# Performance work log

Hardware: AMD Instinct MI355X
Metric: run time of the kernel (lower is better)

## Reference

```python
import jax, jax.numpy as jnp
import numpy as np


def _lstm_cell(x, h, c, w_ih, w_hh, b_ih, b_hh):
    # PyTorch LSTMCell gate order: i, f, g, o
    z = x @ w_ih.T + h @ w_hh.T + b_ih + b_hh
    i, f, g, o = jnp.split(z, 4, axis=-1)
    c_new = jax.nn.sigmoid(f) * c + jax.nn.sigmoid(i) * jnp.tanh(g)
    h_new = jax.nn.sigmoid(o) * jnp.tanh(c_new)
    return h_new, c_new


def setup_inputs() -> dict:
    B, T_in, T_out = 32, 512, 512
    n_mel, n_frames = 80, 1
    n_enc, n_att, n_filt, K = 512, 128, 32, 31
    n_arnn, n_drnn, n_pre = 1024, 1024, 256
    keys = jax.random.split(jax.random.key(0), 25)
    r = lambda k, *s: jax.random.normal(keys[k], s, dtype=jnp.float32) * 0.05
    return {
        "memory": jax.random.normal(keys[0], (B, T_in, n_enc), dtype=jnp.float32),
        "decoder_inputs": jax.random.normal(keys[1], (B, n_mel, T_out), dtype=jnp.float32),
        "memory_lengths": jax.random.randint(keys[2], (B,), T_in // 2, T_in + 1).astype(jnp.int32),
        "prenet_w1": r(3, n_pre, n_mel * n_frames),
        "prenet_w2": r(4, n_pre, n_pre),
        "arnn_w_ih": r(5, 4 * n_arnn, n_pre + n_enc),
        "arnn_w_hh": r(6, 4 * n_arnn, n_arnn),
        "arnn_b_ih": r(7, 4 * n_arnn),
        "arnn_b_hh": r(8, 4 * n_arnn),
        "query_w": r(9, n_att, n_arnn),
        "memory_w": r(10, n_att, n_enc),
        "v_w": r(11, 1, n_att),
        "loc_conv_w": r(12, n_filt, 2, K),
        "loc_dense_w": r(13, n_att, n_filt),
        "drnn_w_ih": r(14, 4 * n_drnn, n_arnn + n_enc),
        "drnn_w_hh": r(15, 4 * n_drnn, n_drnn),
        "drnn_b_ih": r(16, 4 * n_drnn),
        "drnn_b_hh": r(17, 4 * n_drnn),
        "proj_w": r(18, n_mel * n_frames, n_drnn + n_enc),
        "proj_b": r(19, n_mel * n_frames),
        "gate_w": r(20, 1, n_drnn + n_enc),
        "gate_b": r(21, 1),
    }


def reference(memory, decoder_inputs, memory_lengths, prenet_w1, prenet_w2,
              arnn_w_ih, arnn_w_hh, arnn_b_ih, arnn_b_hh,
              query_w, memory_w, v_w, loc_conv_w, loc_dense_w,
              drnn_w_ih, drnn_w_hh, drnn_b_ih, drnn_b_hh,
              proj_w, proj_b, gate_w, gate_b):
    B, T_in, n_enc = memory.shape
    n_mel, T_out = decoder_inputs.shape[1], decoder_inputs.shape[2]
    n_arnn = arnn_w_hh.shape[1]
    n_drnn = drnn_w_hh.shape[1]
    K = loc_conv_w.shape[-1]
    dt = memory.dtype

    # mask: True = padded position (masked_fill with -inf in torch)
    mask = jnp.arange(T_in)[None, :] >= memory_lengths[:, None]          # (B, T_in)
    processed_memory = memory @ memory_w.T                               # (B, T_in, n_att)

    # teacher-forced inputs with go frame: (T_out+1, B, n_mel)
    go = jnp.zeros((1, B, n_mel), dt)
    dec_in = jnp.concatenate([go, jnp.transpose(decoder_inputs, (2, 0, 1))], 0)
    # prenet (dropout omitted for a deterministic reference)
    pre = jax.nn.relu(dec_in @ prenet_w1.T)
    pre = jax.nn.relu(pre @ prenet_w2.T)[:-1]                            # (T_out, B, n_pre)

    init = (jnp.zeros((B, n_arnn), dt), jnp.zeros((B, n_arnn), dt),
            jnp.zeros((B, n_drnn), dt), jnp.zeros((B, n_drnn), dt),
            jnp.zeros((B, T_in), dt), jnp.zeros((B, T_in), dt),
            jnp.zeros((B, n_enc), dt))

    def step(carry, pre_t):
        ah, ac, dh, dc, aw, aw_cum, actx = carry
        # attention RNN
        ah, ac = _lstm_cell(jnp.concatenate([pre_t, actx], -1), ah, ac,
                            arnn_w_ih, arnn_w_hh, arnn_b_ih, arnn_b_hh)
        # location-sensitive attention
        aw_cat = jnp.stack([aw, aw_cum], axis=1)                         # (B, 2, T_in)
        loc = jax.lax.conv_general_dilated(
            aw_cat, loc_conv_w, (1,), [(K // 2, K // 2)],
            dimension_numbers=("NCH", "OIH", "NCH"))                   # (B, n_filt, T_in)
        loc = jnp.transpose(loc, (0, 2, 1)) @ loc_dense_w.T              # (B, T_in, n_att)
        pq = (ah @ query_w.T)[:, None, :]                                # (B, 1, n_att)
        e = (jnp.tanh(pq + loc + processed_memory) @ v_w.T)[..., 0]      # (B, T_in)
        e = jnp.where(mask, -jnp.inf, e)
        aw = jax.nn.softmax(e, axis=1)
        actx = jnp.einsum("bt,bte->be", aw, memory)                      # (B, n_enc)
        aw_cum = aw_cum + aw
        # decoder RNN
        dh, dc = _lstm_cell(jnp.concatenate([ah, actx], -1), dh, dc,
                            drnn_w_ih, drnn_w_hh, drnn_b_ih, drnn_b_hh)
        dhc = jnp.concatenate([dh, actx], -1)
        mel = dhc @ proj_w.T + proj_b
        gate = (dhc @ gate_w.T + gate_b)[:, 0]
        return (ah, ac, dh, dc, aw, aw_cum, actx), (mel, gate, aw)

    _, (mels, gates, aligns) = jax.lax.scan(step, init, pre)
    mel_outputs = jnp.transpose(mels, (1, 2, 0))        # (B, n_mel, T_out)
    gate_outputs = gates.T                              # (B, T_out)
    alignments = jnp.transpose(aligns, (1, 0, 2))       # (B, T_out, T_in)
    return mel_outputs, gate_outputs, alignments
```

## Files before the change

### kernel.cpp

```cpp
#include <hip/hip_runtime.h>
#include <math.h>

#define NB 32
#define TIN 512
#define TOUT 512
#define NENC 512
#define NATT 128
#define NU 1024
#define NG 4096
#define NPRE 256
#define NMEL 80

#define WS_AH    0u
#define WS_AC    32768u
#define WS_DH    65536u
#define WS_DC    98304u
#define WS_ACTX  131072u
#define WS_AW    147456u
#define WS_AWCUM 163840u
#define WS_E     180224u
#define WS_PQ    196608u
#define WS_ZD    200704u
#define WS_ZA    2822144u
#define WS_PM    4657152u
#define WS_PRE   6754304u
#define WS_STATE_ZERO_BYTES (200704u * 4u)
#define OUT_ALIGN ((size_t)NB * NMEL * TOUT + (size_t)NB * TOUT)

__device__ __forceinline__ float fsigm(float x) { return 1.f / (1.f + __expf(-x)); }
__device__ __forceinline__ float ftanh(float x) { return 1.f - 2.f / (__expf(2.f * x) + 1.f); }

__global__ __launch_bounds__(256) void prenet1_kernel(const float* __restrict__ dec,
                                                      const float* __restrict__ w1,
                                                      float* __restrict__ pre) {
    int t = blockIdx.x;
    __shared__ float xl[NB][NMEL];
    for (int i = threadIdx.x; i < NB * NMEL; i += 256) {
        int b = i / NMEL, m = i % NMEL;
        xl[b][m] = (t == 0) ? 0.0f : dec[(b * NMEL + m) * TOUT + (t - 1)];
    }
    __syncthreads();
    int j = threadIdx.x;
    float acc[NB];
#pragma unroll
    for (int b = 0; b < NB; b++) acc[b] = 0.0f;
    for (int m = 0; m < NMEL; m++) {
        float w = w1[j * NMEL + m];
#pragma unroll
        for (int b = 0; b < NB; b++) acc[b] += xl[b][m] * w;
    }
    for (int b = 0; b < NB; b++) pre[((size_t)t * NB + b) * NPRE + j] = fmaxf(acc[b], 0.0f);
}

__global__ __launch_bounds__(256) void prenet2_kernel(const float* __restrict__ w2,
                                                      float* __restrict__ pre) {
    int t = blockIdx.x;
    __shared__ float hl[NB][NPRE];
    for (int i = threadIdx.x; i < NB * NPRE; i += 256)
        hl[i / NPRE][i % NPRE] = pre[(size_t)t * NB * NPRE + i];
    __syncthreads();
    int j = threadIdx.x;
    float acc[NB];
#pragma unroll
    for (int b = 0; b < NB; b++) acc[b] = 0.0f;
    for (int k = 0; k < NPRE; k++) {
        float w = w2[j * NPRE + k];
#pragma unroll
        for (int b = 0; b < NB; b++) acc[b] += hl[b][k] * w;
    }
    for (int b = 0; b < NB; b++) pre[((size_t)t * NB + b) * NPRE + j] = fmaxf(acc[b], 0.0f);
}

__global__ __launch_bounds__(128) void pm_kernel(const float* __restrict__ mem,
                                                 const float* __restrict__ mw,
                                                 float* __restrict__ pm) {
    int b = blockIdx.y, t0 = blockIdx.x * 4;
    __shared__ float ml[4][NENC];
    for (int i = threadIdx.x; i < 4 * NENC; i += 128)
        ml[i / NENC][i % NENC] = mem[((size_t)b * TIN + t0 + i / NENC) * NENC + (i % NENC)];
    __syncthreads();
    int a = threadIdx.x;
    float acc[4] = {0, 0, 0, 0};
    for (int e = 0; e < NENC; e++) {
        float w = mw[a * NENC + e];
#pragma unroll
        for (int tt = 0; tt < 4; tt++) acc[tt] += ml[tt][e] * w;
    }
    for (int tt = 0; tt < 4; tt++)
        pm[((size_t)b * TIN + t0 + tt) * NATT + a] = acc[tt];
}

__global__ __launch_bounds__(256) void z_fused_kernel(
        const float* __restrict__ dwih, const float* __restrict__ dwhh,
        const float* __restrict__ awih, const float* __restrict__ awhh,
        const float* __restrict__ ws_base, const float* __restrict__ pre_t,
        float* __restrict__ zd, float* __restrict__ za, int sbase) {
    int col = blockIdx.x * 256 + threadIdx.x;
    int s = blockIdx.y + sbase;
    const float* ah   = ws_base + WS_AH;
    const float* dh   = ws_base + WS_DH;
    const float* actx = ws_base + WS_ACTX;
    const float* W; const float* x; int xs;
    if (s < 8)       { W = dwih + (size_t)col * 1536 + s * 128;              x = ah + s * 128;          xs = NU;   }
    else if (s < 12) { W = dwih + (size_t)col * 1536 + 1024 + (s - 8) * 128; x = actx + (s - 8) * 128;  xs = NENC; }
    else if (s < 20) { W = dwhh + (size_t)col * 1024 + (s - 12) * 128;       x = dh + (s - 12) * 128;   xs = NU;   }
    else if (s < 22) { W = awih + (size_t)col * 768 + (s - 20) * 128;        x = pre_t + (s - 20) * 128; xs = NPRE; }
    else if (s < 26) { W = awih + (size_t)col * 768 + 256 + (s - 22) * 128;  x = actx + (s - 22) * 128; xs = NENC; }
    else             { W = awhh + (size_t)col * 1024 + (s - 26) * 128;       x = ah + (s - 26) * 128;   xs = NU;   }

    float acc[NB];
#pragma unroll
    for (int b = 0; b < NB; b++) acc[b] = 0.0f;
    for (int k4 = 0; k4 < 32; k4++) {
        float4 w4 = *(const float4*)(W + k4 * 4);
#pragma unroll
        for (int b = 0; b < NB; b++) {
            float4 x4 = *(const float4*)(x + (size_t)b * xs + k4 * 4);
            acc[b] = fmaf(w4.x, x4.x, acc[b]);
            acc[b] = fmaf(w4.y, x4.y, acc[b]);
            acc[b] = fmaf(w4.z, x4.z, acc[b]);
            acc[b] = fmaf(w4.w, x4.w, acc[b]);
        }
    }
    float* zp = ((s < 20) ? (zd + (size_t)s * NB * NG) : (za + (size_t)(s - 20) * NB * NG)) + col;
#pragma unroll
    for (int b = 0; b < NB; b++) zp[(size_t)b * NG] = acc[b];
}

__global__ __launch_bounds__(128) void energies_kernel(const float* __restrict__ pm,
                                                       const float* __restrict__ wc,
                                                       const float* __restrict__ ldw,
                                                       const float* __restrict__ vw,
                                                       const int* __restrict__ mlen,
                                                       const float* __restrict__ ws_aw,
                                                       const float* __restrict__ ws_awcum,
                                                       const float* __restrict__ ws_pq,
                                                       float* __restrict__ ws_e) {
    int b = blockIdx.y, tc = blockIdx.x;
    int tt = threadIdx.x & 31, sub = threadIdx.x >> 5;
    int t = tc * 32 + tt;
    __shared__ float awl[TIN], cuml[TIN], locl[32][33], pql[NATT], ep[32][4];
    for (int i = threadIdx.x; i < TIN; i += 128) {
        awl[i]  = ws_aw[b * TIN + i];
        cuml[i] = ws_awcum[b * TIN + i];
    }
    for (int i = threadIdx.x; i < NATT; i += 128) pql[i] = ws_pq[b * NATT + i];
    __syncthreads();
    for (int f = sub * 8; f < sub * 8 + 8; f++) {
        float s = 0.0f;
        const float* wA = wc + f * 62;
        const float* wB = wA + 31;
        for (int d = 0; d < 31; d++) {
            int tp = t + d - 15;
            if (tp >= 0 && tp < TIN) s += awl[tp] * wA[d] + cuml[tp] * wB[d];
        }
        locl[tt][f] = s;
    }
    __syncthreads();
    float acc = 0.0f;
    const float* pmb = pm + ((size_t)b * TIN + t) * NATT;
    for (int a = sub * 32; a < sub * 32 + 32; a++) {
        float s = pql[a] + pmb[a];
        const float* lw = ldw + a * 32;
#pragma unroll
        for (int f = 0; f < 32; f++) s += locl[tt][f] * lw[f];
        acc += tanhf(s) * vw[a];
    }
    ep[tt][sub] = acc;
    __syncthreads();
    if (sub == 0) {
        float ev = ep[tt][0] + ep[tt][1] + ep[tt][2] + ep[tt][3];
        if (t >= mlen[b]) ev = -3.0e38f;
        ws_e[b * TIN + t] = ev;
    }
}

__global__ __launch_bounds__(256) void softmax_ctx_kernel(const float* __restrict__ mem,
                                                          const float* __restrict__ E,
                                                          float* __restrict__ AW,
                                                          float* __restrict__ AWCUM,
                                                          float* __restrict__ ACTX,
                                                          float* __restrict__ out_align, int step) {
    int b = blockIdx.y, ec = blockIdx.x;
    __shared__ float el[TIN];
    __shared__ float red[256];
    __shared__ float part[4][64];
    const float* Eb = E + b * TIN;
    for (int i = threadIdx.x; i < TIN; i += 256) el[i] = Eb[i];
    __syncthreads();
    red[threadIdx.x] = fmaxf(el[threadIdx.x], el[threadIdx.x + 256]);
    __syncthreads();
    for (int s = 128; s > 0; s >>= 1) {
        if (threadIdx.x < s) red[threadIdx.x] = fmaxf(red[threadIdx.x], red[threadIdx.x + s]);
        __syncthreads();
    }
    float mx = red[0];
    __syncthreads();
    float p0 = __expf(el[threadIdx.x] - mx), p1 = __expf(el[threadIdx.x + 256] - mx);
    el[threadIdx.x] = p0; el[threadIdx.x + 256] = p1;
    red[threadIdx.x] = p0 + p1;
    __syncthreads();
    for (int s = 128; s > 0; s >>= 1) {
        if (threadIdx.x < s) red[threadIdx.x] += red[threadIdx.x + s];
        __syncthreads();
    }
    float inv = 1.0f / red[0];
    int ei = ec * 64 + (threadIdx.x & 63), tp4 = threadIdx.x >> 6;
    float acc = 0.0f;
    const float* mb = mem + (size_t)b * TIN * NENC + ei;
    for (int t = tp4 * 128; t < tp4 * 128 + 128; t++) acc += el[t] * mb[(size_t)t * NENC];
    part[tp4][threadIdx.x & 63] = acc;
    __syncthreads();
    if (threadIdx.x < 64) {
        float ctx = (part[0][threadIdx.x] + part[1][threadIdx.x] +
                     part[2][threadIdx.x] + part[3][threadIdx.x]) * inv;
        ACTX[b * NENC + ec * 64 + threadIdx.x] = ctx;
    }
    if (ec == 0) {
        for (int i = threadIdx.x; i < TIN; i += 256) {
            float a_ = el[i] * inv;
            AW[b * TIN + i] = a_;
            AWCUM[b * TIN + i] += a_;
            out_align[((size_t)b * TOUT + step) * TIN + i] = a_;
        }
    }
}

__global__ __launch_bounds__(512) void gates_kernel(
        const float* __restrict__ abih, const float* __restrict__ abhh,
        const float* __restrict__ qw,
        const float* __restrict__ dbih, const float* __restrict__ dbhh,
        const float* __restrict__ pjw, const float* __restrict__ pjb,
        const float* __restrict__ gtw, const float* __restrict__ gtb,
        float* __restrict__ ws, float* __restrict__ out, int t) {
    __shared__ float sm[NU + NENC];
    int tid = threadIdx.x, bid = blockIdx.x;
    if (bid < 32) {
        if (t < 0) return;
        int b = bid;
        float* DH = ws + WS_DH + (size_t)b * NU;
        float* DC = ws + WS_DC + (size_t)b * NU;
        for (int u = tid; u < NU; u += 512) {
            float zi = dbih[u]          + dbhh[u];
            float zf = dbih[NU + u]     + dbhh[NU + u];
            float zg = dbih[2 * NU + u] + dbhh[2 * NU + u];
            float zo = dbih[3 * NU + u] + dbhh[3 * NU + u];
            for (int s = 0; s < 20; s++) {
                const float* z = ws + WS_ZD + ((size_t)s * NB + b) * NG;
                zi += z[u]; zf += z[NU + u]; zg += z[2 * NU + u]; zo += z[3 * NU + u];
            }
            float c = fsigm(zf) * DC[u] + fsigm(zi) * ftanh(zg);
            float h = fsigm(zo) * ftanh(c);
            DC[u] = c; DH[u] = h; sm[u] = h;
        }
        for (int i = tid; i < NENC; i += 512) sm[NU + i] = ws[WS_ACTX + b * NENC + i];
        __syncthreads();
        int col = tid >> 2, q = tid & 3;
        if (col < 81) {
            const float* wr = (col < 80) ? (pjw + (size_t)col * 1536) : gtw;
            const float* d4 = sm + q * 384;
            const float* w4 = wr + q * 384;
            float s = 0.f;
#pragma unroll
            for (int k4 = 0; k4 < 96; k4++) {
                float4 hv = *(const float4*)(d4 + k4 * 4);
                float4 wv = *(const float4*)(w4 + k4 * 4);
                s = fmaf(hv.x, wv.x, s); s = fmaf(hv.y, wv.y, s);
                s = fmaf(hv.z, wv.z, s); s = fmaf(hv.w, wv.w, s);
            }
            s += __shfl_xor(s, 1); s += __shfl_xor(s, 2);
            if (q == 0) {
                s += (col < 80) ? pjb[col] : gtb[0];
                if (col < 80) out[((size_t)b * NMEL + col) * TOUT + t] = s;
                else          out[(size_t)NB * NMEL * TOUT + (size_t)b * TOUT + t] = s;
            }
        }
    } else {
        int b = bid - 32;
        float* AH = ws + WS_AH + (size_t)b * NU;
        float* AC = ws + WS_AC + (size_t)b * NU;
        for (int u = tid; u < NU; u += 512) {
            float zi = abih[u]          + abhh[u];
            float zf = abih[NU + u]     + abhh[NU + u];
            float zg = abih[2 * NU + u] + abhh[2 * NU + u];
            float zo = abih[3 * NU + u] + abhh[3 * NU + u];
            for (int s = 0; s < 14; s++) {
                const float* z = ws + WS_ZA + ((size_t)s * NB + b) * NG;
                zi += z[u]; zf += z[NU + u]; zg += z[2 * NU + u]; zo += z[3 * NU + u];
            }
            float c = fsigm(zf) * AC[u] + fsigm(zi) * ftanh(zg);
            float h = fsigm(zo) * ftanh(c);
            AC[u] = c; AH[u] = h; sm[u] = h;
        }
        __syncthreads();
        int a = tid >> 2, q = tid & 3;
        if (a < NATT) {
            const float* qr = qw + (size_t)a * NU + q * 256;
            const float* h4 = sm + q * 256;
            float s = 0.f;
#pragma unroll
            for (int k4 = 0; k4 < 64; k4++) {
                float4 hv = *(const float4*)(h4 + k4 * 4);
                float4 wv = *(const float4*)(qr + k4 * 4);
                s = fmaf(hv.x, wv.x, s); s = fmaf(hv.y, wv.y, s);
                s = fmaf(hv.z, wv.z, s); s = fmaf(hv.w, wv.w, s);
            }
            s += __shfl_xor(s, 1); s += __shfl_xor(s, 2);
            if (q == 0) ws[WS_PQ + b * NATT + a] = s;
        }
    }
}

extern "C" void kernel_launch(void* const* d_in, const int* in_sizes, int n_in,
                              void* d_out, int out_size, void* d_ws, size_t ws_size,
                              hipStream_t stream) {
    const float* memory = (const float*)d_in[0];
    const float* dec    = (const float*)d_in[1];
    const int*   mlen   = (const int*)d_in[2];
    const float* pw1    = (const float*)d_in[3];
    const float* pw2    = (const float*)d_in[4];
    const float* awih   = (const float*)d_in[5];
    const float* awhh   = (const float*)d_in[6];
    const float* abih   = (const float*)d_in[7];
    const float* abhh   = (const float*)d_in[8];
    const float* qw     = (const float*)d_in[9];
    const float* mw     = (const float*)d_in[10];
    const float* vw     = (const float*)d_in[11];
    const float* wc     = (const float*)d_in[12];
    const float* ldw    = (const float*)d_in[13];
    const float* dwih   = (const float*)d_in[14];
    const float* dwhh   = (const float*)d_in[15];
    const float* dbih   = (const float*)d_in[16];
    const float* dbhh   = (const float*)d_in[17];
    const float* pjw    = (const float*)d_in[18];
    const float* pjb    = (const float*)d_in[19];
    const float* gtw    = (const float*)d_in[20];
    const float* gtb    = (const float*)d_in[21];
    float* ws  = (float*)d_ws;
    float* out = (float*)d_out;
    float* out_align = out + OUT_ALIGN;

    hipMemsetAsync(ws, 0, WS_STATE_ZERO_BYTES, stream);
    hipMemsetAsync(ws + WS_PRE + (size_t)512 * NB * NPRE, 0, (size_t)NB * NPRE * 4, stream);

    prenet1_kernel<<<TOUT, 256, 0, stream>>>(dec, pw1, ws + WS_PRE);
    prenet2_kernel<<<TOUT, 256, 0, stream>>>(pw2, ws + WS_PRE);
    pm_kernel<<<dim3(TIN / 4, NB), 128, 0, stream>>>(memory, mw, ws + WS_PM);

    z_fused_kernel<<<dim3(16, 14), 256, 0, stream>>>(
        dwih, dwhh, awih, awhh, ws, ws + WS_PRE, ws + WS_ZD, ws + WS_ZA, 20);
    gates_kernel<<<64, 512, 0, stream>>>(abih, abhh, qw, dbih, dbhh, pjw, pjb,
                                         gtw, gtb, ws, out, -1);

    for (int t = 0; t < TOUT; ++t) {
        energies_kernel<<<dim3(16, NB), 128, 0, stream>>>(
            ws + WS_PM, wc, ldw, vw, mlen,
            ws + WS_AW, ws + WS_AWCUM, ws + WS_PQ, ws + WS_E);
        softmax_ctx_kernel<<<dim3(8, NB), 256, 0, stream>>>(
            memory, ws + WS_E, ws + WS_AW, ws + WS_AWCUM, ws + WS_ACTX, out_align, t);
        z_fused_kernel<<<dim3(16, 34), 256, 0, stream>>>(
            dwih, dwhh, awih, awhh, ws,
            ws + WS_PRE + (size_t)(t + 1) * NB * NPRE,
            ws + WS_ZD, ws + WS_ZA, 0);
        gates_kernel<<<64, 512, 0, stream>>>(abih, abhh, qw, dbih, dbhh, pjw, pjb,
                                             gtw, gtb, ws, out, t);
    }
}
```

Baseline: 96.13 ms.

## Fuse attention energies, softmax and context into one block overlapped with z slices

Merges the per-step energies and softmax/context kernels into a single per-batch block. That block runs in the same launch as the z-matrix slices that do not depend on the new attention context. The context-dependent slices move to a separate small kernel. Processed memory is stored transposed so each thread reads its time index coalesced, and location features are kept in registers. This cuts launches per step and overlaps attention with the independent GEMV work. The cost is that all attention work for a batch row now runs serially in one block, which may lengthen the critical path.

```diff
diff --git a/kernel.cpp b/kernel.cpp
--- a/kernel.cpp
+++ b/kernel.cpp
@@ -71,9 +71,9 @@
     for (int b = 0; b < NB; b++) pre[((size_t)t * NB + b) * NPRE + j] = fmaxf(acc[b], 0.0f);
 }
 
-__global__ __launch_bounds__(128) void pm_kernel(const float* __restrict__ mem,
-                                                 const float* __restrict__ mw,
-                                                 float* __restrict__ pm) {
+__global__ __launch_bounds__(128) void pmt_kernel(const float* __restrict__ mem,
+                                                  const float* __restrict__ mw,
+                                                  float* __restrict__ pmt) {
     int b = blockIdx.y, t0 = blockIdx.x * 4;
     __shared__ float ml[4][NENC];
     for (int i = threadIdx.x; i < 4 * NENC; i += 128)
@@ -86,27 +86,24 @@
 #pragma unroll
         for (int tt = 0; tt < 4; tt++) acc[tt] += ml[tt][e] * w;
     }
-    for (int tt = 0; tt < 4; tt++)
-        pm[((size_t)b * TIN + t0 + tt) * NATT + a] = acc[tt];
-}
-
-__global__ __launch_bounds__(256) void z_fused_kernel(
+    *(float4*)&pmt[((size_t)b * NATT + a) * TIN + t0] = make_float4(acc[0], acc[1], acc[2], acc[3]);
+}
+
+__device__ __forceinline__ void z_slice_body(
         const float* __restrict__ dwih, const float* __restrict__ dwhh,
         const float* __restrict__ awih, const float* __restrict__ awhh,
         const float* __restrict__ ws_base, const float* __restrict__ pre_t,
-        float* __restrict__ zd, float* __restrict__ za, int sbase) {
-    int col = blockIdx.x * 256 + threadIdx.x;
-    int s = blockIdx.y + sbase;
+        float* __restrict__ zd, float* __restrict__ za, int s, int col) {
     const float* ah   = ws_base + WS_AH;
     const float* dh   = ws_base + WS_DH;
     const float* actx = ws_base + WS_ACTX;
     const float* W; const float* x; int xs;
-    if (s < 8)       { W = dwih + (size_t)col * 1536 + s * 128;              x = ah + s * 128;          xs = NU;   }
-    else if (s < 12) { W = dwih + (size_t)col * 1536 + 1024 + (s - 8) * 128; x = actx + (s - 8) * 128;  xs = NENC; }
-    else if (s < 20) { W = dwhh + (size_t)col * 1024 + (s - 12) * 128;       x = dh + (s - 12) * 128;   xs = NU;   }
+    if (s < 8)       { W = dwih + (size_t)col * 1536 + s * 128;              x = ah + s * 128;           xs = NU;   }
+    else if (s < 12) { W = dwih + (size_t)col * 1536 + 1024 + (s - 8) * 128; x = actx + (s - 8) * 128;   xs = NENC; }
+    else if (s < 20) { W = dwhh + (size_t)col * 1024 + (s - 12) * 128;       x = dh + (s - 12) * 128;    xs = NU;   }
     else if (s < 22) { W = awih + (size_t)col * 768 + (s - 20) * 128;        x = pre_t + (s - 20) * 128; xs = NPRE; }
-    else if (s < 26) { W = awih + (size_t)col * 768 + 256 + (s - 22) * 128;  x = actx + (s - 22) * 128; xs = NENC; }
-    else             { W = awhh + (size_t)col * 1024 + (s - 26) * 128;       x = ah + (s - 26) * 128;   xs = NU;   }
+    else if (s < 26) { W = awih + (size_t)col * 768 + 256 + (s - 22) * 128;  x = actx + (s - 22) * 128;  xs = NENC; }
+    else             { W = awhh + (size_t)col * 1024 + (s - 26) * 128;       x = ah + (s - 26) * 128;    xs = NU;   }
 
     float acc[NB];
 #pragma unroll
@@ -127,103 +124,108 @@
     for (int b = 0; b < NB; b++) zp[(size_t)b * NG] = acc[b];
 }
 
-__global__ __launch_bounds__(128) void energies_kernel(const float* __restrict__ pm,
-                                                       const float* __restrict__ wc,
-                                                       const float* __restrict__ ldw,
-                                                       const float* __restrict__ vw,
-                                                       const int* __restrict__ mlen,
-                                                       const float* __restrict__ ws_aw,
-                                                       const float* __restrict__ ws_awcum,
-                                                       const float* __restrict__ ws_pq,
-                                                       float* __restrict__ ws_e) {
-    int b = blockIdx.y, tc = blockIdx.x;
-    int tt = threadIdx.x & 31, sub = threadIdx.x >> 5;
-    int t = tc * 32 + tt;
-    __shared__ float awl[TIN], cuml[TIN], locl[32][33], pql[NATT], ep[32][4];
-    for (int i = threadIdx.x; i < TIN; i += 128) {
-        awl[i]  = ws_aw[b * TIN + i];
-        cuml[i] = ws_awcum[b * TIN + i];
-    }
-    for (int i = threadIdx.x; i < NATT; i += 128) pql[i] = ws_pq[b * NATT + i];
-    __syncthreads();
-    for (int f = sub * 8; f < sub * 8 + 8; f++) {
-        float s = 0.0f;
-        const float* wA = wc + f * 62;
-        const float* wB = wA + 31;
-        for (int d = 0; d < 31; d++) {
-            int tp = t + d - 15;
-            if (tp >= 0 && tp < TIN) s += awl[tp] * wA[d] + cuml[tp] * wB[d];
-        }
-        locl[tt][f] = s;
-    }
-    __syncthreads();
-    float acc = 0.0f;
-    const float* pmb = pm + ((size_t)b * TIN + t) * NATT;
-    for (int a = sub * 32; a < sub * 32 + 32; a++) {
-        float s = pql[a] + pmb[a];
-        const float* lw = ldw + a * 32;
-#pragma unroll
-        for (int f = 0; f < 32; f++) s += locl[tt][f] * lw[f];
-        acc += tanhf(s) * vw[a];
-    }
-    ep[tt][sub] = acc;
-    __syncthreads();
-    if (sub == 0) {
-        float ev = ep[tt][0] + ep[tt][1] + ep[tt][2] + ep[tt][3];
-        if (t >= mlen[b]) ev = -3.0e38f;
-        ws_e[b * TIN + t] = ev;
-    }
-}
-
-__global__ __launch_bounds__(256) void softmax_ctx_kernel(const float* __restrict__ mem,
-                                                          const float* __restrict__ E,
-                                                          float* __restrict__ AW,
-                                                          float* __restrict__ AWCUM,
-                                                          float* __restrict__ ACTX,
-                                                          float* __restrict__ out_align, int step) {
-    int b = blockIdx.y, ec = blockIdx.x;
-    __shared__ float el[TIN];
-    __shared__ float red[256];
-    __shared__ float part[4][64];
-    const float* Eb = E + b * TIN;
-    for (int i = threadIdx.x; i < TIN; i += 256) el[i] = Eb[i];
-    __syncthreads();
-    red[threadIdx.x] = fmaxf(el[threadIdx.x], el[threadIdx.x + 256]);
-    __syncthreads();
-    for (int s = 128; s > 0; s >>= 1) {
-        if (threadIdx.x < s) red[threadIdx.x] = fmaxf(red[threadIdx.x], red[threadIdx.x + s]);
-        __syncthreads();
-    }
-    float mx = red[0];
-    __syncthreads();
-    float p0 = __expf(el[threadIdx.x] - mx), p1 = __expf(el[threadIdx.x + 256] - mx);
-    el[threadIdx.x] = p0; el[threadIdx.x + 256] = p1;
-    red[threadIdx.x] = p0 + p1;
-    __syncthreads();
-    for (int s = 128; s > 0; s >>= 1) {
-        if (threadIdx.x < s) red[threadIdx.x] += red[threadIdx.x + s];
-        __syncthreads();
-    }
-    float inv = 1.0f / red[0];
-    int ei = ec * 64 + (threadIdx.x & 63), tp4 = threadIdx.x >> 6;
-    float acc = 0.0f;
-    const float* mb = mem + (size_t)b * TIN * NENC + ei;
-    for (int t = tp4 * 128; t < tp4 * 128 + 128; t++) acc += el[t] * mb[(size_t)t * NENC];
-    part[tp4][threadIdx.x & 63] = acc;
-    __syncthreads();
-    if (threadIdx.x < 64) {
-        float ctx = (part[0][threadIdx.x] + part[1][threadIdx.x] +
-                     part[2][threadIdx.x] + part[3][threadIdx.x]) * inv;
-        ACTX[b * NENC + ec * 64 + threadIdx.x] = ctx;
-    }
-    if (ec == 0) {
-        for (int i = threadIdx.x; i < TIN; i += 256) {
-            float a_ = el[i] * inv;
-            AW[b * TIN + i] = a_;
-            AWCUM[b * TIN + i] += a_;
-            out_align[((size_t)b * TOUT + step) * TIN + i] = a_;
-        }
-    }
+__device__ void attn_body(const float* __restrict__ memory, const int* __restrict__ mlen,
+                          const float* __restrict__ wc, const float* __restrict__ ldw,
+                          const float* __restrict__ vw,
+                          float* __restrict__ ws, float* __restrict__ out_align,
+                          int b, int step, int tid, float* sm) {
+    float* awl = sm, *cuml = sm + 512, *pql = sm + 1024, *red = sm + 1152;
+    awl[tid]  = ws[WS_AW + b * 512 + tid];
+    cuml[tid] = ws[WS_AWCUM + b * 512 + tid];
+    if (tid < NATT) pql[tid] = ws[WS_PQ + b * NATT + tid];
+    __syncthreads();
+    int t = tid;
+    float loc[32];
+#pragma unroll
+    for (int f = 0; f < 32; ++f) loc[f] = 0.f;
+    for (int d = 0; d < 31; ++d) {
+        int tp = t + d - 15;
+        int tc = min(max(tp, 0), 511);
+        bool ok = (tp >= 0) && (tp < 512);
+        float a_ = ok ? awl[tc] : 0.f;
+        float c_ = ok ? cuml[tc] : 0.f;
+#pragma unroll
+        for (int f = 0; f < 32; ++f)
+            loc[f] = fmaf(a_, wc[f * 62 + d], fmaf(c_, wc[f * 62 + 31 + d], loc[f]));
+    }
+    float e = 0.f;
+    const float* pmt = ws + WS_PM + (size_t)b * NATT * TIN + t;
+    for (int a = 0; a < NATT; ++a) {
+        float s = pql[a] + pmt[(size_t)a * TIN];
+#pragma unroll
+        for (int f = 0; f < 32; ++f) s = fmaf(loc[f], ldw[a * 32 + f], s);
+        e = fmaf(ftanh(s), vw[a], e);
+    }
+    if (t >= mlen[b]) e = -3.0e38f;
+    float m = e;
+#pragma unroll
+    for (int sh = 1; sh <= 32; sh <<= 1) m = fmaxf(m, __shfl_xor(m, sh));
+    if ((tid & 63) == 0) red[tid >> 6] = m;
+    __syncthreads();
+    m = fmaxf(fmaxf(fmaxf(red[0], red[1]), fmaxf(red[2], red[3])),
+              fmaxf(fmaxf(red[4], red[5]), fmaxf(red[6], red[7])));
+    float pv = __expf(e - m);
+    float ss = pv;
+#pragma unroll
+    for (int sh = 1; sh <= 32; sh <<= 1) ss += __shfl_xor(ss, sh);
+    if ((tid & 63) == 0) red[8 + (tid >> 6)] = ss;
+    __syncthreads();
+    float tot = red[8] + red[9] + red[10] + red[11] + red[12] + red[13] + red[14] + red[15];
+    float aw = pv / tot;
+    ws[WS_AW + b * 512 + t] = aw;
+    ws[WS_AWCUM + b * 512 + t] += aw;
+    out_align[((size_t)b * TOUT + step) * TIN + t] = aw;
+    __syncthreads();
+    awl[tid] = aw;
+    __syncthreads();
+    const float* mb = memory + (size_t)b * TIN * NENC + tid;
+    float a0 = 0.f, a1 = 0.f, a2 = 0.f, a3 = 0.f;
+    for (int tt = 0; tt < TIN; tt += 4) {
+        a0 = fmaf(awl[tt],     mb[(size_t)tt * NENC], a0);
+        a1 = fmaf(awl[tt + 1], mb[(size_t)(tt + 1) * NENC], a1);
+        a2 = fmaf(awl[tt + 2], mb[(size_t)(tt + 2) * NENC], a2);
+        a3 = fmaf(awl[tt + 3], mb[(size_t)(tt + 3) * NENC], a3);
+    }
+    ws[WS_ACTX + b * NENC + tid] = (a0 + a1) + (a2 + a3);
+}
+
+__global__ __launch_bounds__(512) void attn_zmain_kernel(
+        const float* __restrict__ dwih, const float* __restrict__ dwhh,
+        const float* __restrict__ awih, const float* __restrict__ awhh,
+        const float* __restrict__ memory, const int* __restrict__ mlen,
+        const float* __restrict__ wc, const float* __restrict__ ldw,
+        const float* __restrict__ vw,
+        float* __restrict__ ws, float* __restrict__ out_align,
+        const float* __restrict__ pre_t1, int step) {
+    __shared__ float sm[1168];
+    int tid = threadIdx.x, bid = blockIdx.x;
+    if (bid < 208) {
+        int sidx = bid >> 3;
+        int s = sidx + (sidx < 8 ? 0 : (sidx < 18 ? 4 : 8));
+        z_slice_body(dwih, dwhh, awih, awhh, ws, pre_t1,
+                     ws + WS_ZD, ws + WS_ZA, s, (bid & 7) * 512 + tid);
+    } else {
+        attn_body(memory, mlen, wc, ldw, vw, ws, out_align, bid - 208, step, tid, sm);
+    }
+}
+
+__global__ __launch_bounds__(512) void zactx_kernel(
+        const float* __restrict__ dwih, const float* __restrict__ dwhh,
+        const float* __restrict__ awih, const float* __restrict__ awhh,
+        float* __restrict__ ws) {
+    int sidx = blockIdx.x >> 3;
+    int s = sidx + (sidx < 4 ? 8 : 18);
+    z_slice_body(dwih, dwhh, awih, awhh, ws, ws + WS_PRE,
+                 ws + WS_ZD, ws + WS_ZA, s, ((int)blockIdx.x & 7) * 512 + (int)threadIdx.x);
+}
+
+__global__ __launch_bounds__(512) void za_prologue_kernel(
+        const float* __restrict__ dwih, const float* __restrict__ dwhh,
+        const float* __restrict__ awih, const float* __restrict__ awhh,
+        float* __restrict__ ws) {
+    int s = 20 + ((int)blockIdx.x >> 3);
+    z_slice_body(dwih, dwhh, awih, awhh, ws, ws + WS_PRE,
+                 ws + WS_ZD, ws + WS_ZA, s, ((int)blockIdx.x & 7) * 512 + (int)threadIdx.x);
 }
 
 __global__ __launch_bounds__(512) void gates_kernel(
@@ -345,23 +347,17 @@
 
     prenet1_kernel<<<TOUT, 256, 0, stream>>>(dec, pw1, ws + WS_PRE);
     prenet2_kernel<<<TOUT, 256, 0, stream>>>(pw2, ws + WS_PRE);
-    pm_kernel<<<dim3(TIN / 4, NB), 128, 0, stream>>>(memory, mw, ws + WS_PM);
-
-    z_fused_kernel<<<dim3(16, 14), 256, 0, stream>>>(
-        dwih, dwhh, awih, awhh, ws, ws + WS_PRE, ws + WS_ZD, ws + WS_ZA, 20);
+    pmt_kernel<<<dim3(TIN / 4, NB), 128, 0, stream>>>(memory, mw, ws + WS_PM);
+
+    za_prologue_kernel<<<112, 512, 0, stream>>>(dwih, dwhh, awih, awhh, ws);
     gates_kernel<<<64, 512, 0, stream>>>(abih, abhh, qw, dbih, dbhh, pjw, pjb,
                                          gtw, gtb, ws, out, -1);
 
     for (int t = 0; t < TOUT; ++t) {
-        energies_kernel<<<dim3(16, NB), 128, 0, stream>>>(
-            ws + WS_PM, wc, ldw, vw, mlen,
-            ws + WS_AW, ws + WS_AWCUM, ws + WS_PQ, ws + WS_E);
-        softmax_ctx_kernel<<<dim3(8, NB), 256, 0, stream>>>(
-            memory, ws + WS_E, ws + WS_AW, ws + WS_AWCUM, ws + WS_ACTX, out_align, t);
-        z_fused_kernel<<<dim3(16, 34), 256, 0, stream>>>(
-            dwih, dwhh, awih, awhh, ws,
-            ws + WS_PRE + (size_t)(t + 1) * NB * NPRE,
-            ws + WS_ZD, ws + WS_ZA, 0);
+        attn_zmain_kernel<<<240, 512, 0, stream>>>(
+            dwih, dwhh, awih, awhh, memory, mlen, wc, ldw, vw,
+            ws, out_align, ws + WS_PRE + (size_t)(t + 1) * NB * NPRE, t);
+        zactx_kernel<<<64, 512, 0, stream>>>(dwih, dwhh, awih, awhh, ws);
         gates_kernel<<<64, 512, 0, stream>>>(abih, abhh, qw, dbih, dbhh, pjw, pjb,
                                              gtw, gtb, ws, out, t);
     }
```

Measured after the change: 112.2 ms. 16.7% more time.
